# Kernel tuning notes

Measured on AMD Instinct MI355X. Metric: run time of the kernel, lower is better.

The kernel has to match this reference:

```python
import jax, jax.numpy as jnp
import numpy as np
from jax import lax

DIM = 192
HEADS = 8
B, H, W = 8, 128, 128


def dwconv3x3(x, w):
    # x: [B,C,H,W], w: [C,1,3,3] depthwise (groups=C)
    return lax.conv_general_dilated(
        x, w, window_strides=(1, 1), padding='SAME',
        feature_group_count=x.shape[1],
        dimension_numbers=('NCHW', 'OIHW', 'NCHW'))


def conv1x1(x, w, b=None):
    # w: [Cout, Cin]
    y = jnp.einsum('oc,bchw->bohw', w, x)
    if b is not None:
        y = y + b[None, :, None, None]
    return y


def setup_inputs() -> dict:
    key = jax.random.key(0)
    ks = jax.random.split(key, 9)
    s = 0.02
    return {
        'x': jax.random.normal(ks[0], (B, DIM, H, W), jnp.float32),
        'w_qkv': jax.random.normal(ks[1], (3 * DIM, DIM), jnp.float32) * s,
        'b_qkv': jnp.zeros((3 * DIM,), jnp.float32),
        'w_dw': jax.random.normal(ks[2], (3 * DIM, 1, 3, 3), jnp.float32) * s,
        'b_dw': jnp.zeros((3 * DIM,), jnp.float32),
        'w_proj': jax.random.normal(ks[3], (DIM, DIM), jnp.float32) * s,
        'b_proj': jnp.zeros((DIM,), jnp.float32),
        'w_pos1': jax.random.normal(ks[4], (DIM, 1, 3, 3), jnp.float32) * s,
        'w_pos2': jax.random.normal(ks[5], (DIM, 1, 3, 3), jnp.float32) * s,
        'temperature': jnp.ones((HEADS, 1, 1), jnp.float32),
    }


def reference(x, w_qkv, b_qkv, w_dw, b_dw, w_proj, b_proj, w_pos1, w_pos2, temperature):
    b, c, h, w = x.shape
    heads = HEADS
    ch = c // heads

    qkv = conv1x1(x, w_qkv, b_qkv)
    qkv = dwconv3x3(qkv, w_dw) + b_dw[None, :, None, None]
    q_inp, k_inp, v_inp = jnp.split(qkv, 3, axis=1)

    def to_heads(t):  # [B,C,H,W] -> [B,heads,ch,HW]
        return t.reshape(b, heads, ch, h * w)

    q = to_heads(q_inp)
    k = to_heads(k_inp)
    v = to_heads(v_inp)

    # L2 normalize over hw (torch F.normalize, eps=1e-12)
    q = q / jnp.maximum(jnp.linalg.norm(q, axis=-1, keepdims=True), 1e-12)
    k = k / jnp.maximum(jnp.linalg.norm(k, axis=-1, keepdims=True), 1e-12)

    attn = jnp.einsum('bhce,bhde->bhcd', q, k) * temperature  # [B,heads,ch,ch]
    attn = jax.nn.softmax(attn, axis=-1)
    out = jnp.einsum('bhcd,bhde->bhce', attn, v)  # [B,heads,ch,HW]
    out = out.reshape(b, c, h, w)

    out = conv1x1(out, w_proj, b_proj)

    pos = dwconv3x3(v_inp, w_pos1)
    pos = jax.nn.gelu(pos, approximate=False)
    pos = dwconv3x3(pos, w_pos2)

    return out + pos
```

## Files before the change

kernel.cpp:

```cpp
#include <hip/hip_runtime.h>
#include <stdint.h>
#include <stddef.h>

#define NB 8
#define CC 192
#define C3 576
#define HGT 128
#define WID 128
#define HW 16384
#define NH 8
#define QKROW 49152

typedef short bf16x8 __attribute__((ext_vector_type(8)));
typedef float f32x4 __attribute__((ext_vector_type(4)));

__device__ __forceinline__ unsigned short f2bf(float f) {
  unsigned int u = __float_as_uint(f);
  u += 0x7fffu + ((u >> 16) & 1u);
  return (unsigned short)(u >> 16);
}
__device__ __forceinline__ float bf2f(unsigned short h) {
  return __uint_as_float(((unsigned int)h) << 16);
}
__device__ __forceinline__ float bflo(unsigned int v) {
  return __uint_as_float(v << 16);
}
__device__ __forceinline__ float bfhi(unsigned int v) {
  return __uint_as_float(v & 0xffff0000u);
}
__device__ __forceinline__ unsigned int pk2(float a, float b) {
  return (unsigned int)f2bf(a) | ((unsigned int)f2bf(b) << 16);
}
__device__ __forceinline__ void gl_lds16(const void* g, void* l) {
  __builtin_amdgcn_global_load_lds(
      (const __attribute__((address_space(1))) unsigned int*)(uintptr_t)g,
      (__attribute__((address_space(3))) unsigned int*)(uint32_t)(uintptr_t)l,
      16, 0, 0);
}
__device__ __forceinline__ int xcd_swz(int g, int n) {
  return (g & 7) * (n >> 3) + (g >> 3);
}

__global__ __launch_bounds__(256) void ktrans(const float* __restrict__ x,
                                              unsigned char* __restrict__ xT) {
  __shared__ __align__(16) float lx[192 * 68];
  int wg = xcd_swz(blockIdx.x, gridDim.x);
  int pt = wg & 255, b = wg >> 8;
  int p0 = pt * 64;
  int tid = threadIdx.x;
#pragma unroll
  for (int i = 0; i < 12; ++i) {
    int f = tid + i * 256;
    int ic = f >> 4, q = f & 15;
    float4 v = *(const float4*)(x + ((size_t)(b * CC + ic)) * HW + p0 + q * 4);
    *(float4*)(lx + ic * 68 + q * 4) = v;
  }
  __syncthreads();
#pragma unroll
  for (int i = 0; i < 6; ++i) {
    int f = i * 256 + tid;
    int s = f >> 6, p = f & 63;
    unsigned int wv[4];
#pragma unroll
    for (int j = 0; j < 4; ++j)
      wv[j] = pk2(lx[(s * 8 + 2 * j) * 68 + p], lx[(s * 8 + 2 * j + 1) * 68 + p]);
    uint4 st; st.x = wv[0]; st.y = wv[1]; st.z = wv[2]; st.w = wv[3];
    *(uint4*)(xT + (((size_t)(b * 24 + s)) * HW + p0 + p) * 16) = st;
  }
}

__global__ void kwprep(const float* __restrict__ wq, unsigned char* __restrict__ wb) {
  int f = blockIdx.x * 256 + threadIdx.x;
  if (f >= C3 * 24) return;
  int oc = f / 24, s = f % 24;
  unsigned int wv[4];
#pragma unroll
  for (int j = 0; j < 4; ++j)
    wv[j] = pk2(wq[oc * 192 + s * 8 + 2 * j], wq[oc * 192 + s * 8 + 2 * j + 1]);
  uint4 st; st.x = wv[0]; st.y = wv[1]; st.z = wv[2]; st.w = wv[3];
  *(uint4*)(wb + (size_t)oc * 384 + ((s ^ (oc & 7)) * 16)) = st;
}

__global__ __launch_bounds__(256) void kconv1(const unsigned char* __restrict__ xT,
                                              const unsigned char* __restrict__ wb,
                                              const float* __restrict__ bqkv,
                                              unsigned short* __restrict__ vout,
                                              unsigned char* __restrict__ qkout) {
  __shared__ __align__(16) unsigned char lds[73728];
  int wg = xcd_swz(blockIdx.x, gridDim.x);
  int ot = wg % 9; int rest = wg / 9; int grp = rest & 63; int b = rest >> 6;
  int tid = threadIdx.x;
  const unsigned char* gB = wb + (size_t)ot * 24576;
#pragma unroll
  for (int i = 0; i < 6; ++i)
    gl_lds16(gB + i * 4096 + tid * 16, lds + 49152 + i * 4096 + tid * 16);
  const unsigned char* gA = xT + (size_t)b * 24 * HW * 16;
  int t0 = grp * 4;
  {
    int p0 = t0 * 64;
#pragma unroll
    for (int i = 0; i < 6; ++i) {
      int f = i * 256 + tid;
      gl_lds16(gA + (((size_t)(f >> 6)) * HW + p0 + (f & 63)) * 16, lds + f * 16);
    }
  }
  int lane = tid & 63, w = tid >> 6;
  int l15 = lane & 15, gq = lane >> 4;
  int pw = w * 16;
  float bias[4];
  size_t obase[4];
  int isv[4], key[4];
#pragma unroll
  for (int nf = 0; nf < 4; ++nf) {
    int oc = ot * 64 + nf * 16 + l15;
    bias[nf] = bqkv[oc];
    if (oc >= 384) {
      isv[nf] = 1;
      obase[nf] = ((size_t)(b * CC + oc - 384)) * HW * 2;
      key[nf] = 0;
    } else {
      isv[nf] = 0;
      int part = oc >= 192 ? 1 : 0;
      int cm = oc - part * 192;
      obase[nf] = ((size_t)((part * 8 + b) * 128)) * QKROW + cm * 256;
      key[nf] = cm & 7;
    }
  }
  for (int it = 0; it < 4; ++it) {
    int tile = t0 + it;
    asm volatile("s_waitcnt vmcnt(0)" ::: "memory");
    __syncthreads();
    int nb = it & 1;
    if (it < 3) {
      int p1 = (tile + 1) * 64;
#pragma unroll
      for (int i = 0; i < 6; ++i) {
        int f = i * 256 + tid;
        gl_lds16(gA + (((size_t)(f >> 6)) * HW + p1 + (f & 63)) * 16,
                 lds + ((nb ^ 1) * 24576) + f * 16);
      }
    }
    f32x4 acc[4];
#pragma unroll
    for (int nf = 0; nf < 4; ++nf) acc[nf] = (f32x4){0.f, 0.f, 0.f, 0.f};
#pragma unroll
    for (int kk = 0; kk < 6; ++kk) {
      bf16x8 a = *(const bf16x8*)(lds + nb * 24576 + ((((kk * 4 + gq) << 6) + pw + l15) * 16));
      int cb = kk * 64 + gq * 16;
#pragma unroll
      for (int nf = 0; nf < 4; ++nf) {
        int r = nf * 16 + l15;
        bf16x8 bfr = *(const bf16x8*)(lds + 49152 + r * 384 + (cb ^ ((r & 7) << 4)));
        acc[nf] = __builtin_amdgcn_mfma_f32_16x16x32_bf16(a, bfr, acc[nf], 0, 0, 0);
      }
    }
    int p = tile * 64 + pw + gq * 4;
    int y = p >> 7, x = p & 127;
    int u = x >> 3, sub = (x & 7) * 2;
#pragma unroll
    for (int nf = 0; nf < 4; ++nf) {
      uint2 st;
      st.x = pk2(acc[nf][0] + bias[nf], acc[nf][1] + bias[nf]);
      st.y = pk2(acc[nf][2] + bias[nf], acc[nf][3] + bias[nf]);
      if (isv[nf]) {
        *(uint2*)((unsigned char*)vout + obase[nf] + (size_t)p * 2) = st;
      } else {
        *(uint2*)(qkout + obase[nf] + (size_t)y * QKROW + ((u ^ key[nf]) * 16 + sub)) = st;
      }
    }
  }
}

__global__ __launch_bounds__(256) void kqk(const unsigned char* __restrict__ qk,
                                           const float* __restrict__ wdw,
                                           const float* __restrict__ bdw,
                                           float* __restrict__ G,
                                           float* __restrict__ nq,
                                           float* __restrict__ nk) {
  __shared__ __align__(16) unsigned char lds[81920];
  const int FB = 49152;
  int wg = xcd_swz(blockIdx.x, gridDim.x);
  int band = wg & 63, h = (wg >> 6) & 7, b = wg >> 9;
  int y0 = band * 2;
  int tid = threadIdx.x;
#pragma unroll
  for (int i = 0; i < 12; ++i) {
    int f = i * 256 + tid;
    int p = f / 1536, rem = f % 1536;
    int r = rem / 384, u = rem % 384;
    int y = y0 - 1 + r;
    if (y >= 0 && y < HGT)
      gl_lds16(qk + ((size_t)((p * 8 + b) * 128 + y)) * QKROW + h * 6144 + u * 16,
               lds + f * 16);
    else
      *(uint4*)(lds + f * 16) = (uint4){0, 0, 0, 0};
  }
  asm volatile("s_waitcnt vmcnt(0)" ::: "memory");
  __syncthreads();

  int lane = tid & 63, w = tid >> 6;
  if (tid < 192) {
    int p = tid / 96; int r3m = tid % 96;
    int ch = r3m >> 2; int row = (r3m >> 1) & 1; int half = r3m & 1;
    int gc = p * 192 + h * 24 + ch;
    float wv[9];
#pragma unroll
    for (int j = 0; j < 9; ++j) wv[j] = wdw[gc * 9 + j];
    float bias = bdw[gc];
    const unsigned char* sbase = lds + p * 24576 + ch * 256;
    int ckey = ch & 7;
    unsigned char* fb = lds + FB + p * 16384 + ch * 16;
    int h8 = half * 8;
    unsigned int W[3][16];
#define LOADU(dy_, m_, u_) { \
    uint4 tt = ((u_) >= 0 && (u_) < 16) \
        ? *(const uint4*)(sbase + (row + (dy_)) * 6144 + (((u_) ^ ckey) * 16)) \
        : (uint4){0, 0, 0, 0}; \
    W[dy_][(m_) * 4 + 0] = tt.x; W[dy_][(m_) * 4 + 1] = tt.y; \
    W[dy_][(m_) * 4 + 2] = tt.z; W[dy_][(m_) * 4 + 3] = tt.w; }
#pragma unroll
    for (int dy = 0; dy < 3; ++dy) {
#pragma unroll
      for (int m = 0; m < 4; ++m) { LOADU(dy, m, h8 - 1 + m); }
    }
    float nsum = 0.f;
#pragma unroll
    for (int c4 = 0; c4 < 4; ++c4) {
      if (c4 > 0) {
#pragma unroll
        for (int dy = 0; dy < 3; ++dy) {
#pragma unroll
          for (int e = 0; e < 8; ++e) W[dy][e] = W[dy][8 + e];
          LOADU(dy, 2, h8 - 1 + c4 * 2 + 2);
          LOADU(dy, 3, h8 - 1 + c4 * 2 + 3);
        }
      }
      float acc[16];
#pragma unroll
      for (int j = 0; j < 16; ++j) acc[j] = bias;
#pragma unroll
      for (int dy = 0; dy < 3; ++dy) {
        float f[18];
#pragma unroll
        for (int t2 = 0; t2 < 18; ++t2) {
          int rel = 7 + t2;
          unsigned int v = W[dy][rel >> 1];
          f[t2] = (rel & 1) ? bfhi(v) : bflo(v);
        }
#pragma unroll
        for (int j = 0; j < 16; ++j)
          acc[j] += f[j] * wv[dy * 3] + f[j + 1] * wv[dy * 3 + 1] + f[j + 2] * wv[dy * 3 + 2];
      }
#pragma unroll
      for (int j = 0; j < 16; ++j) nsum += acc[j] * acc[j];
      unsigned int pk[8];
#pragma unroll
      for (int e = 0; e < 8; ++e) pk[e] = pk2(acc[2 * e], acc[2 * e + 1]);
      int kt = row * 4 + half * 2 + (c4 >> 1);
      int gb = (c4 & 1) * 2;
      uint4 s0; s0.x = pk[0]; s0.y = pk[1]; s0.z = pk[2]; s0.w = pk[3];
      uint4 s1; s1.x = pk[4]; s1.y = pk[5]; s1.z = pk[6]; s1.w = pk[7];
      *(uint4*)(fb + kt * 2048 + gb * 512) = s0;
      *(uint4*)(fb + kt * 2048 + (gb + 1) * 512) = s1;
    }
#undef LOADU
    nsum += __shfl_xor(nsum, 1);
    nsum += __shfl_xor(nsum, 2);
    if ((tid & 3) == 0) {
      float* dst = (p == 0) ? nq : nk;
      atomicAdd(dst + (b * NH + h) * 24 + ch, nsum);
    }
  } else {
    int t2 = tid - 192;
#pragma unroll
    for (int i = 0; i < 8; ++i) {
      int f = i * 64 + t2;
      int ch8 = f & 7, gq4 = (f >> 3) & 3, kt8 = (f >> 5) & 7, pp = f >> 8;
      *(uint4*)(lds + FB + pp * 16384 + kt8 * 2048 + gq4 * 512 + (24 + ch8) * 16) =
          (uint4){0, 0, 0, 0};
    }
  }
  __syncthreads();

  int l15 = lane & 15, gq = lane >> 4;
  f32x4 acc2[2][2];
#pragma unroll
  for (int ct = 0; ct < 2; ++ct)
#pragma unroll
    for (int dt = 0; dt < 2; ++dt) acc2[ct][dt] = (f32x4){0.f, 0.f, 0.f, 0.f};
#pragma unroll
  for (int t2 = 0; t2 < 2; ++t2) {
    int kt = w * 2 + t2;
    bf16x8 aq[2], bk[2];
#pragma unroll
    for (int ct = 0; ct < 2; ++ct) {
      aq[ct] = *(const bf16x8*)(lds + FB + kt * 2048 + gq * 512 + (ct * 16 + l15) * 16);
      bk[ct] = *(const bf16x8*)(lds + FB + 16384 + kt * 2048 + gq * 512 + (ct * 16 + l15) * 16);
    }
#pragma unroll
    for (int ct = 0; ct < 2; ++ct)
#pragma unroll
      for (int dt = 0; dt < 2; ++dt)
        acc2[ct][dt] = __builtin_amdgcn_mfma_f32_16x16x32_bf16(aq[ct], bk[dt], acc2[ct][dt], 0, 0, 0);
  }
  float* gp = (float*)lds;
#pragma unroll
  for (int ct = 0; ct < 2; ++ct)
#pragma unroll
    for (int dt = 0; dt < 2; ++dt)
      *(f32x4*)(gp + (((w * 4 + ct * 2 + dt) * 64) + lane) * 4) = acc2[ct][dt];
  __syncthreads();
  float* Gb = G + (size_t)(b * NH + h) * 576;
#pragma unroll
  for (int ii = 0; ii < 3; ++ii) {
    int f = ii * 256 + tid;
    if (f < 576) {
      int c = f / 24, d = f % 24;
      int t4 = ((c >> 4) << 1) + (d >> 4);
      int lane16 = (d & 15) + (((c & 15) >> 2) << 4);
      int reg = c & 3;
      float s = 0.f;
#pragma unroll
      for (int w4 = 0; w4 < 4; ++w4)
        s += gp[((w4 * 4 + t4) * 64 + lane16) * 4 + reg];
      atomicAdd(Gb + f, s);
    }
  }
}

__global__ __launch_bounds__(256) void kdwv(const unsigned short* __restrict__ src,
                                            const float* __restrict__ wdw,
                                            const float* __restrict__ bdw,
                                            unsigned char* __restrict__ vT) {
  __shared__ __align__(16) unsigned int smem[8 * 721];
  int wg = xcd_swz(blockIdx.x, gridDim.x);
  int cg = wg % 24, rt = (wg / 24) & 15, b = wg / 384;
  int y0 = rt * 8, chg0 = cg * 8;
  int tid = threadIdx.x;
  for (int i = tid; i < 5768; i += 256) smem[i] = 0;
  __syncthreads();
#pragma unroll
  for (int i = 0; i < 5; ++i) {
    int f = i * 256 + tid;
    int ch = f / 160, rem = f % 160;
    int r = rem >> 4, seg = rem & 15;
    int y = y0 - 1 + r;
    if (y >= 0 && y < HGT) {
      uint4 v = *(const uint4*)(src + ((size_t)(b * CC + chg0 + ch)) * HW + y * WID + seg * 8);
      unsigned int* dp = smem + ch * 721 + r * 72 + 4 + seg * 4;
      dp[0] = v.x; dp[1] = v.y; dp[2] = v.z; dp[3] = v.w;
    }
  }
  __syncthreads();
  int ch = tid >> 5, u = tid & 31;
  int row = u >> 2, xs = (u & 3) * 32;
  int gch = 384 + chg0 + ch;
  float wv[9];
#pragma unroll
  for (int j = 0; j < 9; ++j) wv[j] = wdw[gch * 9 + j];
  float bias = bdw[gch];
  float outv[32];
  const unsigned int* tb = smem + ch * 721;
#pragma unroll
  for (int g = 0; g < 4; ++g) {
    int x0 = xs + g * 8;
    float v[3][12];
#pragma unroll
    for (int dy = 0; dy < 3; ++dy) {
      const unsigned int* rp = tb + (row + dy) * 72 + ((x0 + 6) >> 1);
#pragma unroll
      for (int m = 0; m < 6; ++m) {
        unsigned int w2 = rp[m];
        v[dy][2 * m] = bf2f((unsigned short)(w2 & 0xffff));
        v[dy][2 * m + 1] = bf2f((unsigned short)(w2 >> 16));
      }
    }
#pragma unroll
    for (int j = 0; j < 8; ++j) {
      float a = bias;
#pragma unroll
      for (int dy = 0; dy < 3; ++dy)
#pragma unroll
        for (int dx = 0; dx < 3; ++dx)
          a += v[dy][j + dx + 1] * wv[dy * 3 + dx];
      outv[g * 8 + j] = a;
    }
  }
  __syncthreads();
  unsigned short* vt = (unsigned short*)smem;
#pragma unroll
  for (int g = 0; g < 4; ++g)
#pragma unroll
    for (int j = 0; j < 8; j += 2) {
      int x = xs + g * 8 + j;
      ((unsigned int*)smem)[ch * 512 + row * 64 + (x >> 1)] =
          pk2(outv[g * 8 + j], outv[g * 8 + j + 1]);
    }
  __syncthreads();
#pragma unroll
  for (int i = 0; i < 4; ++i) {
    int f = i * 256 + tid;
    int r = f >> 7, col = f & 127;
    unsigned int wvp[4];
#pragma unroll
    for (int e = 0; e < 4; ++e) {
      unsigned short a = vt[(2 * e) * 1024 + r * 128 + col];
      unsigned short bb = vt[(2 * e + 1) * 1024 + r * 128 + col];
      wvp[e] = (unsigned int)a | ((unsigned int)bb << 16);
    }
    uint4 st; st.x = wvp[0]; st.y = wvp[1]; st.z = wvp[2]; st.w = wvp[3];
    *(uint4*)(vT + (((size_t)(b * 24 + cg)) * HW + (size_t)(y0 + r) * WID + col) * 16) = st;
  }
}

__global__ __launch_bounds__(256) void kattn(const float* __restrict__ G,
                                             const float* __restrict__ nq,
                                             const float* __restrict__ nk,
                                             const float* __restrict__ temp,
                                             const float* __restrict__ wproj,
                                             unsigned char* __restrict__ W2) {
  __shared__ float attn[24][24];
  __shared__ float iq[24], ik[24];
  int bh = blockIdx.x;
  int h = bh & 7, b = bh >> 3;
  int tid = threadIdx.x;
  const float* Gb = G + (size_t)bh * 576;
  if (tid < 24) { float n = sqrtf(nq[bh * 24 + tid]); iq[tid] = 1.f / fmaxf(n, 1e-12f); }
  else if (tid < 48) { float n = sqrtf(nk[bh * 24 + tid - 24]); ik[tid - 24] = 1.f / fmaxf(n, 1e-12f); }
  __syncthreads();
  if (tid < 24) {
    float tmp = temp[h];
    float row[24];
    float mx = -1e30f;
#pragma unroll
    for (int d = 0; d < 24; ++d) {
      row[d] = Gb[tid * 24 + d] * iq[tid] * ik[d] * tmp;
      mx = fmaxf(mx, row[d]);
    }
    float sum = 0.f;
#pragma unroll
    for (int d = 0; d < 24; ++d) { float e = expf(row[d] - mx); row[d] = e; sum += e; }
    float inv = 1.f / sum;
#pragma unroll
    for (int d = 0; d < 24; ++d) attn[tid][d] = row[d] * inv;
  }
  __syncthreads();
  for (int i = 0; i < 18; ++i) {
    int f = tid + i * 256;
    if (f >= 4608) break;
    int oc = f / 24, d = f % 24;
    float s = 0.f;
#pragma unroll
    for (int c = 0; c < 24; ++c) s += wproj[oc * 192 + h * 24 + c] * attn[c][d];
    int gg = h * 24 + d;
    *(unsigned short*)(W2 + ((size_t)b * CC + oc) * 384 + ((gg * 2) ^ ((oc & 7) << 4))) = f2bf(s);
  }
}

__global__ __launch_bounds__(256) void kpos(const unsigned char* __restrict__ vT,
                                            const float* __restrict__ w1,
                                            const float* __restrict__ w2,
                                            unsigned short* __restrict__ pos) {
  __shared__ unsigned int vbuf[8 * 865];
  __shared__ unsigned int d1[8 * 721];
  int wg = xcd_swz(blockIdx.x, gridDim.x);
  int cg = wg % 24, rt = (wg / 24) & 15, b = wg / 384;
  int y0 = rt * 8, g0 = cg * 8;
  int tid = threadIdx.x;
  for (int i = tid; i < 6920; i += 256) vbuf[i] = 0;
  __syncthreads();
#pragma unroll
  for (int i = 0; i < 3; ++i) {
    int f = i * 256 + tid;
    int r = f >> 6, colp = f & 63;
    int y = y0 - 2 + r;
    if (y >= 0 && y < HGT) {
      const unsigned char* base = vT + (((size_t)(b * 24 + cg)) * HW + (size_t)y * WID + colp * 2) * 16;
      uint4 va = *(const uint4*)(base);
      uint4 vb2 = *(const uint4*)(base + 16);
      unsigned int la[4] = {va.x, va.y, va.z, va.w};
      unsigned int lb[4] = {vb2.x, vb2.y, vb2.z, vb2.w};
#pragma unroll
      for (int e = 0; e < 8; ++e) {
        unsigned int a16 = (la[e >> 1] >> ((e & 1) * 16)) & 0xffff;
        unsigned int b16 = (lb[e >> 1] >> ((e & 1) * 16)) & 0xffff;
        vbuf[e * 865 + r * 72 + colp + 4] = a16 | (b16 << 16);
      }
    }
  }
  __syncthreads();
  int ch = tid >> 5, u = tid & 31;
  {
    const float* wp = w1 + (g0 + ch) * 9;
    float wl[9];
#pragma unroll
    for (int j = 0; j < 9; ++j) wl[j] = wp[j];
    int x0 = u * 4;
    for (int rr = 0; rr < 10; ++rr) {
      int y = y0 - 1 + rr;
      unsigned int o0 = 0, o1 = 0;
      if (y >= 0 && y < HGT) {
        float v[3][8];
#pragma unroll
        for (int dy = 0; dy < 3; ++dy) {
          const unsigned int* rp = vbuf + ch * 865 + (rr + dy) * 72 + ((x0 + 6) >> 1);
#pragma unroll
          for (int m = 0; m < 4; ++m) {
            unsigned int w2r = rp[m];
            v[dy][2 * m] = bf2f((unsigned short)(w2r & 0xffff));
            v[dy][2 * m + 1] = bf2f((unsigned short)(w2r >> 16));
          }
        }
        float g4[4];
#pragma unroll
        for (int j = 0; j < 4; ++j) {
          float a = 0.f;
#pragma unroll
          for (int dy = 0; dy < 3; ++dy)
#pragma unroll
            for (int dx = 0; dx < 3; ++dx)
              a += v[dy][j + dx + 1] * wl[dy * 3 + dx];
          g4[j] = 0.5f * a * (1.f + erff(a * 0.70710678118f));
        }
        o0 = pk2(g4[0], g4[1]);
        o1 = pk2(g4[2], g4[3]);
      }
      unsigned int* dp = d1 + ch * 721 + rr * 72 + ((x0 + 8) >> 1);
      dp[0] = o0; dp[1] = o1;
    }
  }
  if (tid < 160) {
    int ech = tid / 20, rem = tid % 20;
    int rr = rem >> 1, side = rem & 1;
    int x = side ? 128 : -1;
    int y = y0 - 1 + rr;
    unsigned short val = 0;
    if (y >= 0 && y < HGT) {
      const float* wp = w1 + (g0 + ech) * 9;
      float a = 0.f;
      const unsigned short* vb16 = (const unsigned short*)(vbuf + ech * 865);
#pragma unroll
      for (int dy = 0; dy < 3; ++dy)
#pragma unroll
        for (int dx = 0; dx < 3; ++dx)
          a += bf2f(vb16[(rr + dy) * 144 + (x + dx + 7)]) * wp[dy * 3 + dx];
      val = f2bf(0.5f * a * (1.f + erff(a * 0.70710678118f)));
    }
    ((unsigned short*)(d1 + ech * 721))[rr * 144 + (x + 8)] = val;
  }
  __syncthreads();
  {
    const float* wp = w2 + (g0 + ch) * 9;
    float wl[9];
#pragma unroll
    for (int j = 0; j < 9; ++j) wl[j] = wp[j];
    int row = u >> 2, xs = (u & 3) * 32;
    size_t rb = ((size_t)(b * CC + g0 + ch)) * HW + (size_t)(y0 + row) * WID;
#pragma unroll
    for (int g = 0; g < 4; ++g) {
      int x0 = xs + g * 8;
      float v[3][12];
#pragma unroll
      for (int dy = 0; dy < 3; ++dy) {
        const unsigned int* rp = d1 + ch * 721 + (row + dy) * 72 + ((x0 + 6) >> 1);
#pragma unroll
        for (int m = 0; m < 6; ++m) {
          unsigned int w2r = rp[m];
          v[dy][2 * m] = bf2f((unsigned short)(w2r & 0xffff));
          v[dy][2 * m + 1] = bf2f((unsigned short)(w2r >> 16));
        }
      }
      uint4 st;
      float o[8];
#pragma unroll
      for (int j = 0; j < 8; ++j) {
        float a = 0.f;
#pragma unroll
        for (int dy = 0; dy < 3; ++dy)
#pragma unroll
          for (int dx = 0; dx < 3; ++dx)
            a += v[dy][j + dx + 1] * wl[dy * 3 + dx];
        o[j] = a;
      }
      st.x = pk2(o[0], o[1]); st.y = pk2(o[2], o[3]);
      st.z = pk2(o[4], o[5]); st.w = pk2(o[6], o[7]);
      *(uint4*)(pos + rb + x0) = st;
    }
  }
}

__global__ __launch_bounds__(256) void kproj(const unsigned char* __restrict__ vT,
                                             const unsigned char* __restrict__ W2,
                                             const float* __restrict__ bproj,
                                             const unsigned short* __restrict__ pos,
                                             float* __restrict__ out) {
  __shared__ __align__(16) unsigned char lds[73728];
  int wg = xcd_swz(blockIdx.x, gridDim.x);
  int ot = wg % 3; int rest = wg / 3; int grp = rest & 63; int b = rest >> 6;
  int tid = threadIdx.x;
  const unsigned char* gB = W2 + ((size_t)(b * 192 + ot * 64)) * 384;
#pragma unroll
  for (int i = 0; i < 6; ++i)
    gl_lds16(gB + i * 4096 + tid * 16, lds + 49152 + i * 4096 + tid * 16);
  const unsigned char* gA = vT + (size_t)b * 24 * HW * 16;
  int t0 = grp * 4;
  {
    int p0 = t0 * 64;
#pragma unroll
    for (int i = 0; i < 6; ++i) {
      int f = i * 256 + tid;
      gl_lds16(gA + (((size_t)(f >> 6)) * HW + p0 + (f & 63)) * 16, lds + f * 16);
    }
  }
  int lane = tid & 63, w = tid >> 6;
  int l15 = lane & 15, gq = lane >> 4;
  int pw = w * 16;
  float bias[4];
  size_t obase[4];
#pragma unroll
  for (int nf = 0; nf < 4; ++nf) {
    int oc = ot * 64 + nf * 16 + l15;
    bias[nf] = bproj[oc];
    obase[nf] = ((size_t)(b * 192 + oc)) * HW;
  }
  for (int it = 0; it < 4; ++it) {
    int tile = t0 + it;
    asm volatile("s_waitcnt vmcnt(0)" ::: "memory");
    __syncthreads();
    int nb = it & 1;
    if (it < 3) {
      int p1 = (tile + 1) * 64;
#pragma unroll
      for (int i = 0; i < 6; ++i) {
        int f = i * 256 + tid;
        gl_lds16(gA + (((size_t)(f >> 6)) * HW + p1 + (f & 63)) * 16,
                 lds + ((nb ^ 1) * 24576) + f * 16);
      }
    }
    f32x4 acc[4];
#pragma unroll
    for (int nf = 0; nf < 4; ++nf) acc[nf] = (f32x4){0.f, 0.f, 0.f, 0.f};
#pragma unroll
    for (int kk = 0; kk < 6; ++kk) {
      bf16x8 a = *(const bf16x8*)(lds + nb * 24576 + ((((kk * 4 + gq) << 6) + pw + l15) * 16));
      int cb = kk * 64 + gq * 16;
#pragma unroll
      for (int nf = 0; nf < 4; ++nf) {
        int r = nf * 16 + l15;
        bf16x8 bfr = *(const bf16x8*)(lds + 49152 + r * 384 + (cb ^ ((r & 7) << 4)));
        acc[nf] = __builtin_amdgcn_mfma_f32_16x16x32_bf16(a, bfr, acc[nf], 0, 0, 0);
      }
    }
    int p = tile * 64 + pw + gq * 4;
#pragma unroll
    for (int nf = 0; nf < 4; ++nf) {
      uint2 pv = *(const uint2*)(pos + obase[nf] + p);
      float4 o;
      o.x = acc[nf][0] + bias[nf] + bf2f((unsigned short)(pv.x & 0xffff));
      o.y = acc[nf][1] + bias[nf] + bf2f((unsigned short)(pv.x >> 16));
      o.z = acc[nf][2] + bias[nf] + bf2f((unsigned short)(pv.y & 0xffff));
      o.w = acc[nf][3] + bias[nf] + bf2f((unsigned short)(pv.y >> 16));
      *(float4*)(out + obase[nf] + p) = o;
    }
  }
}

#define OFF_W   ((size_t)0)
#define OFF_G   ((size_t)221184)
#define OFF_NQ  ((size_t)368640)
#define OFF_NK  ((size_t)374784)
#define OFF_W2  ((size_t)380928)
#define OFF_QK  ((size_t)970752)
#define OFF_V   ((size_t)101634048)
#define OFF_XT  ((size_t)151965696)

extern "C" void kernel_launch(void* const* d_in, const int* in_sizes, int n_in,
                              void* d_out, int out_size, void* d_ws, size_t ws_size,
                              hipStream_t stream) {
  const float* x     = (const float*)d_in[0];
  const float* wqkv  = (const float*)d_in[1];
  const float* bqkv  = (const float*)d_in[2];
  const float* wdw   = (const float*)d_in[3];
  const float* bdw   = (const float*)d_in[4];
  const float* wproj = (const float*)d_in[5];
  const float* bproj = (const float*)d_in[6];
  const float* wpos1 = (const float*)d_in[7];
  const float* wpos2 = (const float*)d_in[8];
  const float* temp  = (const float*)d_in[9];
  unsigned char* ws = (unsigned char*)d_ws;

  hipMemsetAsync(ws + OFF_G, 0, 147456 + 6144 + 6144, stream);
  kwprep<<<54, 256, 0, stream>>>(wqkv, ws + OFF_W);
  ktrans<<<2048, 256, 0, stream>>>(x, ws + OFF_XT);
  kconv1<<<4608, 256, 0, stream>>>(ws + OFF_XT, ws + OFF_W, bqkv,
                                   (unsigned short*)(ws + OFF_V), ws + OFF_QK);
  kqk<<<4096, 256, 0, stream>>>(ws + OFF_QK, wdw, bdw, (float*)(ws + OFF_G),
                                (float*)(ws + OFF_NQ), (float*)(ws + OFF_NK));
  kdwv<<<3072, 256, 0, stream>>>((const unsigned short*)(ws + OFF_V), wdw, bdw,
                                 ws + OFF_XT);
  kattn<<<64, 256, 0, stream>>>((const float*)(ws + OFF_G), (const float*)(ws + OFF_NQ),
                                (const float*)(ws + OFF_NK), temp, wproj, ws + OFF_W2);
  kpos<<<3072, 256, 0, stream>>>(ws + OFF_XT, wpos1, wpos2,
                                 (unsigned short*)(ws + OFF_QK));
  kproj<<<1536, 256, 0, stream>>>(ws + OFF_XT, ws + OFF_W2, bproj,
                                  (const unsigned short*)(ws + OFF_QK), (float*)d_out);
}
```

Baseline: 329.9 us.

## Stage Q/K conv1 outputs through LDS and write channel-interleaved 16-byte units

```diff
diff --git a/kernel.cpp b/kernel.cpp
--- a/kernel.cpp
+++ b/kernel.cpp
@@ -86,7 +86,8 @@
                                               const float* __restrict__ bqkv,
                                               unsigned short* __restrict__ vout,
                                               unsigned char* __restrict__ qkout) {
-  __shared__ __align__(16) unsigned char lds[73728];
+  __shared__ __align__(16) unsigned char lds[81920];
+  const int TRO = 73728;
   int wg = xcd_swz(blockIdx.x, gridDim.x);
   int ot = wg % 9; int rest = wg / 9; int grp = rest & 63; int b = rest >> 6;
   int tid = threadIdx.x;
@@ -107,25 +108,21 @@
   int lane = tid & 63, w = tid >> 6;
   int l15 = lane & 15, gq = lane >> 4;
   int pw = w * 16;
+  int part = ot / 3, cm0 = (ot % 3) * 64;
+  bool isq = (ot < 6);
   float bias[4];
-  size_t obase[4];
-  int isv[4], key[4];
-#pragma unroll
-  for (int nf = 0; nf < 4; ++nf) {
-    int oc = ot * 64 + nf * 16 + l15;
-    bias[nf] = bqkv[oc];
-    if (oc >= 384) {
-      isv[nf] = 1;
-      obase[nf] = ((size_t)(b * CC + oc - 384)) * HW * 2;
-      key[nf] = 0;
-    } else {
-      isv[nf] = 0;
-      int part = oc >= 192 ? 1 : 0;
-      int cm = oc - part * 192;
-      obase[nf] = ((size_t)((part * 8 + b) * 128)) * QKROW + cm * 256;
-      key[nf] = cm & 7;
-    }
-  }
+#pragma unroll
+  for (int nf = 0; nf < 4; ++nf) bias[nf] = bqkv[ot * 64 + nf * 16 + l15];
+  size_t vbase[4];
+  if (!isq) {
+#pragma unroll
+    for (int nf = 0; nf < 4; ++nf)
+      vbase[nf] = ((size_t)(b * CC + cm0 + nf * 16 + l15)) * HW * 2;
+  }
+  unsigned char* qkbase = qkout + ((size_t)((part * 8 + b) * 128)) * QKROW;
+  int unitw = w * 2 + (gq >> 1);
+  int sub8 = (gq & 1) * 8;
+
   for (int it = 0; it < 4; ++it) {
     int tile = t0 + it;
     asm volatile("s_waitcnt vmcnt(0)" ::: "memory");
@@ -154,18 +151,34 @@
         acc[nf] = __builtin_amdgcn_mfma_f32_16x16x32_bf16(a, bfr, acc[nf], 0, 0, 0);
       }
     }
-    int p = tile * 64 + pw + gq * 4;
-    int y = p >> 7, x = p & 127;
-    int u = x >> 3, sub = (x & 7) * 2;
-#pragma unroll
-    for (int nf = 0; nf < 4; ++nf) {
-      uint2 st;
-      st.x = pk2(acc[nf][0] + bias[nf], acc[nf][1] + bias[nf]);
-      st.y = pk2(acc[nf][2] + bias[nf], acc[nf][3] + bias[nf]);
-      if (isv[nf]) {
-        *(uint2*)((unsigned char*)vout + obase[nf] + (size_t)p * 2) = st;
-      } else {
-        *(uint2*)(qkout + obase[nf] + (size_t)y * QKROW + ((u ^ key[nf]) * 16 + sub)) = st;
+    if (isq) {
+#pragma unroll
+      for (int nf = 0; nf < 4; ++nf) {
+        int c = nf * 16 + l15;
+        uint2 st;
+        st.x = pk2(acc[nf][0] + bias[nf], acc[nf][1] + bias[nf]);
+        st.y = pk2(acc[nf][2] + bias[nf], acc[nf][3] + bias[nf]);
+        *(uint2*)(lds + TRO + c * 128 + ((unitw ^ (c & 7)) * 16) + sub8) = st;
+      }
+      asm volatile("s_waitcnt lgkmcnt(0)" ::: "memory");
+      __builtin_amdgcn_s_barrier();
+      {
+        int y = tile >> 1, xh = (tile & 1) * 8;
+        int u = tid >> 5, c0 = tid & 31, c1 = c0 + 32;
+        uint4 v0 = *(const uint4*)(lds + TRO + c0 * 128 + ((u ^ (c0 & 7)) * 16));
+        uint4 v1 = *(const uint4*)(lds + TRO + c1 * 128 + ((u ^ (c1 & 7)) * 16));
+        unsigned char* grow = qkbase + (size_t)y * QKROW + (xh + u) * 3072 + cm0 * 16;
+        *(uint4*)(grow + c0 * 16) = v0;
+        *(uint4*)(grow + c1 * 16) = v1;
+      }
+    } else {
+      int p = tile * 64 + pw + gq * 4;
+#pragma unroll
+      for (int nf = 0; nf < 4; ++nf) {
+        uint2 st;
+        st.x = pk2(acc[nf][0] + bias[nf], acc[nf][1] + bias[nf]);
+        st.y = pk2(acc[nf][2] + bias[nf], acc[nf][3] + bias[nf]);
+        *(uint2*)((unsigned char*)vout + vbase[nf] + (size_t)p * 2) = st;
       }
     }
   }
@@ -187,10 +200,11 @@
   for (int i = 0; i < 12; ++i) {
     int f = i * 256 + tid;
     int p = f / 1536, rem = f % 1536;
-    int r = rem / 384, u = rem % 384;
+    int r = rem / 384, unit = rem % 384;
+    int uc = unit / 24, ch = unit % 24;
     int y = y0 - 1 + r;
     if (y >= 0 && y < HGT)
-      gl_lds16(qk + ((size_t)((p * 8 + b) * 128 + y)) * QKROW + h * 6144 + u * 16,
+      gl_lds16(qk + ((size_t)((p * 8 + b) * 128 + y)) * QKROW + uc * 3072 + (h * 24 + ch) * 16,
                lds + f * 16);
     else
       *(uint4*)(lds + f * 16) = (uint4){0, 0, 0, 0};
@@ -207,14 +221,13 @@
 #pragma unroll
     for (int j = 0; j < 9; ++j) wv[j] = wdw[gc * 9 + j];
     float bias = bdw[gc];
-    const unsigned char* sbase = lds + p * 24576 + ch * 256;
-    int ckey = ch & 7;
+    const unsigned char* sbase = lds + p * 24576 + ch * 16;
     unsigned char* fb = lds + FB + p * 16384 + ch * 16;
     int h8 = half * 8;
     unsigned int W[3][16];
 #define LOADU(dy_, m_, u_) { \
     uint4 tt = ((u_) >= 0 && (u_) < 16) \
-        ? *(const uint4*)(sbase + (row + (dy_)) * 6144 + (((u_) ^ ckey) * 16)) \
+        ? *(const uint4*)(sbase + (row + (dy_)) * 6144 + (u_) * 384) \
         : (uint4){0, 0, 0, 0}; \
     W[dy_][(m_) * 4 + 0] = tt.x; W[dy_][(m_) * 4 + 1] = tt.y; \
     W[dy_][(m_) * 4 + 2] = tt.z; W[dy_][(m_) * 4 + 3] = tt.w; }
```

Result: faster. 308.8 us (-6.4%).
